# Optimization experiments

Hardware: AMD Instinct MI355X
Metric: run time of the kernel (lower is better)

Reference implementation:

```python
import jax, jax.numpy as jnp
import numpy as np

NUM_BLOCKS = 100  # original samples at most 100 blocks; ids are in [0, NUM_BLOCKS)
EPS = 1e-8       # F.cosine_similarity default eps (clamps norms from below)


def setup_inputs() -> dict:
    key = jax.random.key(0)
    k1, k2 = jax.random.split(key)
    N, D = 1000000, 128
    z = jax.random.normal(k1, (N, D), dtype=jnp.float32)
    poi_to_road_block = jax.random.randint(k2, (N,), 0, NUM_BLOCKS, dtype=jnp.int32)
    return {"z": z, "poi_to_road_block": poi_to_road_block}


def reference(z, poi_to_road_block):
    N, D = z.shape
    ids = poi_to_road_block
    # per-block counts and sums -> block centers (mean embedding per road block)
    counts = jax.ops.segment_sum(jnp.ones((N,), z.dtype), ids, num_segments=NUM_BLOCKS)  # [B]
    sums = jax.ops.segment_sum(z, ids, num_segments=NUM_BLOCKS)                          # [B, D]
    centers = sums / jnp.maximum(counts, 1.0)[:, None]                                   # [B, D]
    # cosine similarity between each point and its block center
    c = centers[ids]                                                                     # [N, D] gather
    dot = jnp.sum(z * c, axis=-1)                                                        # [N]
    z_norm = jnp.maximum(jnp.sqrt(jnp.sum(z * z, axis=-1)), EPS)
    c_norm = jnp.maximum(jnp.sqrt(jnp.sum(c * c, axis=-1)), EPS)
    cos = dot / (z_norm * c_norm)                                                        # [N]
    # per-block mean cosine, then average (1 - mean_cos) over blocks with >1 member
    cos_sum = jax.ops.segment_sum(cos, ids, num_segments=NUM_BLOCKS)                     # [B]
    mean_cos = cos_sum / jnp.maximum(counts, 1.0)
    valid = counts > 1.0
    total = jnp.sum(jnp.where(valid, 1.0 - mean_cos, 0.0))
    count = jnp.maximum(jnp.sum(valid.astype(z.dtype)), 1.0)
    return total / count
```

## Files before the change

### kernel.cpp

```cpp
#include <hip/hip_runtime.h>
#include <hip/hip_bf16.h>

#define NBLK 100
#define DIM 128
#define EVEC (NBLK * DIM)
#define SLICE (2 * EVEC + NBLK)
#define EPSV 1e-8f
#define SSCALE 4194304.0f
#define NSCALE 16777216.0f
#define INV_SSCALE (1.0f / SSCALE)
#define INV_NSCALE (1.0f / NSCALE)

__global__ __launch_bounds__(1024) void rbc_accum(
    const float4* __restrict__ z4, const int* __restrict__ ids,
    float* __restrict__ ws, int N, int nwaves) {
  __shared__ int lsum[EVEC];
  __shared__ int lnsum[EVEC];
  __shared__ int lcnt[NBLK];
  const int tid = threadIdx.x;
  for (int e = tid; e < EVEC; e += 1024) { lsum[e] = 0; lnsum[e] = 0; }
  if (tid < NBLK) lcnt[tid] = 0;
  __syncthreads();

  const int lane = tid & 63;
  const int q  = lane >> 4;
  const int r  = lane & 15;
  const int qp = q & 1;
  const int w = blockIdx.x * (blockDim.x >> 6) + (tid >> 6);
  const int ngroups = N >> 2;

#define RBC_POINT_BODY(A0, A1, BB)                                           \
  {                                                                          \
    float sq = A0.x * A0.x + A0.y * A0.y + A0.z * A0.z + A0.w * A0.w +       \
               A1.x * A1.x + A1.y * A1.y + A1.z * A1.z + A1.w * A1.w;        \
    _Pragma("unroll")                                                        \
    for (int m = 1; m < 16; m <<= 1) sq += __shfl_xor(sq, m);                \
    const float rn = 1.0f / fmaxf(sqrtf(sq), EPSV);                          \
    const float v0[4] = {A0.x, A0.y, A0.z, A0.w};                            \
    const float v1[4] = {A1.x, A1.y, A1.z, A1.w};                            \
    const int base = BB * DIM;                                               \
    _Pragma("unroll")                                                        \
    for (int s = 0; s < 4; ++s) {                                            \
      const float x0 = qp ? v0[s ^ 1] : v0[s];                               \
      const float x1 = qp ? v1[s ^ 1] : v1[s];                               \
      const int p0 = base + r + ((((s & 1) ^ qp)) << 4) + ((s >> 1) << 5);   \
      atomicAdd(&lsum[p0], __float2int_rn(x0 * SSCALE));                     \
      atomicAdd(&lnsum[p0], __float2int_rn(x0 * rn * NSCALE));               \
      atomicAdd(&lsum[p0 + 64], __float2int_rn(x1 * SSCALE));                \
      atomicAdd(&lnsum[p0 + 64], __float2int_rn(x1 * rn * NSCALE));          \
    }                                                                        \
    if (r == 0) atomicAdd(&lcnt[BB], 1);                                     \
  }

  int j = w;
  for (; j + nwaves < ngroups; j += (nwaves << 1)) {
    const int jB = j + nwaves;
    const int iA = (j << 2) + q;
    const int iB = (jB << 2) + q;
    const float4* zpA = z4 + ((size_t)iA << 5);
    const float4* zpB = z4 + ((size_t)iB << 5);
    const float4 a0 = zpA[r];
    const float4 a1 = zpA[r + 16];
    const float4 b0 = zpB[r];
    const float4 b1 = zpB[r + 16];
    const int bA = ids[iA];
    const int bB = ids[iB];
    RBC_POINT_BODY(a0, a1, bA);
    RBC_POINT_BODY(b0, b1, bB);
  }
  if (j < ngroups) {
    const int iA = (j << 2) + q;
    const float4* zpA = z4 + ((size_t)iA << 5);
    const float4 a0 = zpA[r];
    const float4 a1 = zpA[r + 16];
    const int bA = ids[iA];
    RBC_POINT_BODY(a0, a1, bA);
  }
  if (blockIdx.x == 0 && (tid >> 6) == 0 && (N & 3)) {
    const int i = (ngroups << 2) + q;
    if (q < (N & 3)) {
      const float4* zp = z4 + ((size_t)i << 5);
      const float4 a0 = zp[r];
      const float4 a1 = zp[r + 16];
      const int b = ids[i];
      RBC_POINT_BODY(a0, a1, b);
    }
  }
#undef RBC_POINT_BODY
  __syncthreads();

  float* slice = ws + (size_t)blockIdx.x * SLICE;
  for (int e = tid; e < EVEC; e += 1024) {
    slice[e] = (float)lsum[e] * INV_SSCALE;
    slice[EVEC + e] = (float)lnsum[e] * INV_NSCALE;
  }
  if (tid < NBLK) slice[2 * EVEC + tid] = (float)lcnt[tid];
}

__global__ __launch_bounds__(512) void rbc_blockstat(
    const float* __restrict__ ws, float* __restrict__ stat, int G) {
  __shared__ float sp[512];
  __shared__ float np_[512];
  const int b = blockIdx.x;
  const int t = threadIdx.x;
  const int d = t & 127;
  const int qq = t >> 7;
  const int gpq = (G + 3) >> 2;
  const int g0 = qq * gpq;
  const int g1 = (g0 + gpq < G) ? (g0 + gpq) : G;
  float s = 0.f, n = 0.f;
  for (int g = g0; g < g1; ++g) {
    const float* f = ws + (size_t)g * SLICE + (size_t)b * DIM;
    s += f[d];
    n += f[EVEC + d];
  }
  sp[t] = s;
  np_[t] = n;

  if (t >= 256 && t < 320) {
    const int l = t - 256;
    float c = 0.f;
    for (int g = l; g < G; g += 64) c += ws[(size_t)g * SLICE + 2 * EVEC + b];
#pragma unroll
    for (int m = 1; m < 64; m <<= 1) c += __shfl_xor(c, m);
    if (l == 0) stat[b * 4 + 2] = c;
  }
  __syncthreads();

  if (t < 128) {
    const float ss = sp[t] + sp[t + 128] + sp[t + 256] + sp[t + 384];
    const float nn = np_[t] + np_[t + 128] + np_[t + 256] + np_[t + 384];
    sp[t] = ss * ss;
    np_[t] = nn * ss;
  }
  __syncthreads();

  if (t < 64) {
    float S2 = sp[t] + sp[t + 64];
    float ND = np_[t] + np_[t + 64];
#pragma unroll
    for (int m = 1; m < 64; m <<= 1) {
      S2 += __shfl_xor(S2, m);
      ND += __shfl_xor(ND, m);
    }
    if (t == 0) {
      stat[b * 4 + 0] = ND;
      stat[b * 4 + 1] = S2;
    }
  }
}

__global__ __launch_bounds__(128) void rbc_final(const float* __restrict__ stat,
                                                 float* __restrict__ out) {
  __shared__ float lv[2];
  __shared__ float lc[2];
  const int t = threadIdx.x;
  float val = 0.f, vc = 0.f;
  if (t < NBLK) {
    const float ND = stat[t * 4 + 0];
    const float S2 = stat[t * 4 + 1];
    const float cnt = stat[t * 4 + 2];
    const float cnt1 = fmaxf(cnt, 1.0f);
    const float cn = fmaxf(sqrtf(S2) / cnt1, EPSV);
    const float mean_cos = ND / (cnt1 * cnt1 * cn);
    if (cnt > 1.0f) { val = 1.0f - mean_cos; vc = 1.0f; }
  }
#pragma unroll
  for (int m = 1; m < 64; m <<= 1) {
    val += __shfl_xor(val, m);
    vc += __shfl_xor(vc, m);
  }
  if ((t & 63) == 0) { lv[t >> 6] = val; lc[t >> 6] = vc; }
  __syncthreads();
  if (t == 0) out[0] = (lv[0] + lv[1]) / fmaxf(lc[0] + lc[1], 1.0f);
}

extern "C" void kernel_launch(void* const* d_in, const int* in_sizes, int n_in,
                              void* d_out, int out_size, void* d_ws, size_t ws_size,
                              hipStream_t stream) {
  const float* z = (const float*)d_in[0];
  const int* ids = (const int*)d_in[1];
  const int N = in_sizes[1];
  float* out = (float*)d_out;
  float* ws = (float*)d_ws;

  size_t cap = (ws_size - 400 * sizeof(float)) / (sizeof(float) * (size_t)SLICE);
  int G = 256;
  if (cap < (size_t)G) G = (int)(cap > 1 ? cap : 1);
  const int nwaves = G * (1024 / 64);

  rbc_accum<<<G, 1024, 0, stream>>>((const float4*)z, ids, ws, N, nwaves);

  float* stat = ws + (size_t)G * SLICE;
  rbc_blockstat<<<NBLK, 512, 0, stream>>>(ws, stat, G);
  rbc_final<<<1, 128, 0, stream>>>(stat, out);
}
```

Baseline: 125.0 us.

## Software-pipeline point loads and use DPP reduction with fast rcp/sqrt

Restructures the accumulation loop so the next pair of points' z rows and ids are loaded into registers before the current pair is processed, which is meant to overlap global-memory latency with the LDS atomics. Replaces the shuffle-based 16-lane norm reduction with DPP row operations and uses hardware rcp/sqrt intrinsics, with the norm scale folded into one factor. This raises register pressure at 1024-thread blocks and uses slightly less precise reciprocal and sqrt.

Result: faster. 121.9 us (median of 2 runs) (-2.4%).

```diff
diff --git a/kernel.cpp b/kernel.cpp
--- a/kernel.cpp
+++ b/kernel.cpp
@@ -11,6 +11,23 @@
 #define INV_SSCALE (1.0f / SSCALE)
 #define INV_NSCALE (1.0f / NSCALE)
 
+__device__ __forceinline__ float dpp_qsum16(float x) {
+  int xi, yi;
+  xi = __builtin_bit_cast(int, x);
+  yi = __builtin_amdgcn_update_dpp(0, xi, 0xB1, 0xF, 0xF, false);
+  x += __builtin_bit_cast(float, yi);
+  xi = __builtin_bit_cast(int, x);
+  yi = __builtin_amdgcn_update_dpp(0, xi, 0x4E, 0xF, 0xF, false);
+  x += __builtin_bit_cast(float, yi);
+  xi = __builtin_bit_cast(int, x);
+  yi = __builtin_amdgcn_update_dpp(0, xi, 0x124, 0xF, 0xF, false);
+  x += __builtin_bit_cast(float, yi);
+  xi = __builtin_bit_cast(int, x);
+  yi = __builtin_amdgcn_update_dpp(0, xi, 0x128, 0xF, 0xF, false);
+  x += __builtin_bit_cast(float, yi);
+  return x;
+}
+
 __global__ __launch_bounds__(1024) void rbc_accum(
     const float4* __restrict__ z4, const int* __restrict__ ids,
     float* __restrict__ ws, int N, int nwaves) {
@@ -33,9 +50,10 @@
   {                                                                          \
     float sq = A0.x * A0.x + A0.y * A0.y + A0.z * A0.z + A0.w * A0.w +       \
                A1.x * A1.x + A1.y * A1.y + A1.z * A1.z + A1.w * A1.w;        \
-    _Pragma("unroll")                                                        \
-    for (int m = 1; m < 16; m <<= 1) sq += __shfl_xor(sq, m);                \
-    const float rn = 1.0f / fmaxf(sqrtf(sq), EPSV);                          \
+    sq = dpp_qsum16(sq);                                                     \
+    const float rn =                                                         \
+        __builtin_amdgcn_rcpf(fmaxf(__builtin_amdgcn_sqrtf(sq), EPSV));      \
+    const float rnN = rn * NSCALE;                                           \
     const float v0[4] = {A0.x, A0.y, A0.z, A0.w};                            \
     const float v1[4] = {A1.x, A1.y, A1.z, A1.w};                            \
     const int base = BB * DIM;                                               \
@@ -45,39 +63,50 @@
       const float x1 = qp ? v1[s ^ 1] : v1[s];                               \
       const int p0 = base + r + ((((s & 1) ^ qp)) << 4) + ((s >> 1) << 5);   \
       atomicAdd(&lsum[p0], __float2int_rn(x0 * SSCALE));                     \
-      atomicAdd(&lnsum[p0], __float2int_rn(x0 * rn * NSCALE));               \
+      atomicAdd(&lnsum[p0], __float2int_rn(x0 * rnN));                       \
       atomicAdd(&lsum[p0 + 64], __float2int_rn(x1 * SSCALE));                \
-      atomicAdd(&lnsum[p0 + 64], __float2int_rn(x1 * rn * NSCALE));          \
+      atomicAdd(&lnsum[p0 + 64], __float2int_rn(x1 * rnN));                  \
     }                                                                        \
     if (r == 0) atomicAdd(&lcnt[BB], 1);                                     \
   }
 
-  int j = w;
-  for (; j + nwaves < ngroups; j += (nwaves << 1)) {
-    const int jB = j + nwaves;
-    const int iA = (j << 2) + q;
-    const int iB = (jB << 2) + q;
-    const float4* zpA = z4 + ((size_t)iA << 5);
-    const float4* zpB = z4 + ((size_t)iB << 5);
-    const float4 a0 = zpA[r];
-    const float4 a1 = zpA[r + 16];
-    const float4 b0 = zpB[r];
-    const float4 b1 = zpB[r + 16];
-    const int bA = ids[iA];
-    const int bB = ids[iB];
-    RBC_POINT_BODY(a0, a1, bA);
-    RBC_POINT_BODY(b0, b1, bB);
-  }
-  if (j < ngroups) {
-    const int iA = (j << 2) + q;
-    const float4* zpA = z4 + ((size_t)iA << 5);
-    const float4 a0 = zpA[r];
-    const float4 a1 = zpA[r + 16];
-    const int bA = ids[iA];
-    RBC_POINT_BODY(a0, a1, bA);
+  const int stride2 = nwaves << 1;
+  int j0 = w, j1 = w + nwaves;
+  bool h0 = j0 < ngroups, h1 = j1 < ngroups;
+  float4 A0, A1, B0, B1;
+  int bA = 0, bB = 0;
+  if (h0) {
+    const int i = (j0 << 2) + q;
+    const float4* p = z4 + ((size_t)i << 5);
+    A0 = p[r]; A1 = p[r + 16]; bA = ids[i];
+  }
+  if (h1) {
+    const int i = (j1 << 2) + q;
+    const float4* p = z4 + ((size_t)i << 5);
+    B0 = p[r]; B1 = p[r + 16]; bB = ids[i];
+  }
+  while (h0) {
+    const int n0 = j0 + stride2, n1 = j1 + stride2;
+    const bool hn0 = n0 < ngroups, hn1 = n1 < ngroups;
+    float4 NA0, NA1, NB0, NB1;
+    int nbA = 0, nbB = 0;
+    if (hn0) {
+      const int i = (n0 << 2) + q;
+      const float4* p = z4 + ((size_t)i << 5);
+      NA0 = p[r]; NA1 = p[r + 16]; nbA = ids[i];
+    }
+    if (hn1) {
+      const int i = (n1 << 2) + q;
+      const float4* p = z4 + ((size_t)i << 5);
+      NB0 = p[r]; NB1 = p[r + 16]; nbB = ids[i];
+    }
+    RBC_POINT_BODY(A0, A1, bA);
+    if (h1) RBC_POINT_BODY(B0, B1, bB);
+    A0 = NA0; A1 = NA1; B0 = NB0; B1 = NB1; bA = nbA; bB = nbB;
+    j0 = n0; j1 = n1; h0 = hn0; h1 = hn1;
   }
   if (blockIdx.x == 0 && (tid >> 6) == 0 && (N & 3)) {
-    const int i = (ngroups << 2) + q;
+    const int i = ((ngroups << 2)) + q;
     if (q < (N & 3)) {
       const float4* zp = z4 + ((size_t)i << 5);
       const float4 a0 = zp[r];
```
